# Kernel optimization log

Hardware: AMD Instinct MI355X
Metric: run time of the kernel (lower is better)

## Reference

```python
import jax, jax.numpy as jnp
import numpy as np

B, I, S, H, O = 128, 64, 2048, 128, 64


def setup_inputs() -> dict:
    key = jax.random.key(0)
    ks = jax.random.split(key, 9)
    sc = 0.1
    return {
        "x": jax.random.normal(ks[0], (B, I, S), dtype=jnp.float32),
        "Wx_out": jax.random.normal(ks[1], (I, 4 * H), dtype=jnp.float32) * sc,
        "Wh_out": jax.random.normal(ks[2], (H, 4 * H), dtype=jnp.float32) * sc,
        "b_out": jnp.zeros((4 * H,), dtype=jnp.float32),
        "Wx_in": jax.random.normal(ks[3], (H, 4 * H), dtype=jnp.float32) * sc,
        "Wh_in": jax.random.normal(ks[4], (H, 4 * H), dtype=jnp.float32) * sc,
        "b_in": jnp.zeros((4 * H,), dtype=jnp.float32),
        "W_lin": jax.random.normal(ks[5], (O, H), dtype=jnp.float32) * 0.01,
        "b_lin": jnp.zeros((O,), dtype=jnp.float32),
    }


def reference(x, Wx_out, Wh_out, b_out, Wx_in, Wh_in, b_in, W_lin, b_lin):
    # x: (B, I, S) -> permute(0,2,1) -> (B, S, I); scan over time axis.
    xs = jnp.transpose(x, (2, 0, 1))  # (S, B, I)
    h0 = jnp.zeros((x.shape[0], Wh_out.shape[0]), dtype=x.dtype)

    def step(carry, xt):
        h, c, cn = carry  # outer hidden, outer cell, inner cell
        gates = xt @ Wx_out + h @ Wh_out + b_out
        i, f, o, g = jnp.split(gates, 4, axis=-1)
        i, f, o = jax.nn.sigmoid(i), jax.nn.sigmoid(f), jax.nn.sigmoid(o)
        g = jnp.tanh(g)
        x_in = i * g          # inner LSTM input
        h_in = f * c          # inner LSTM hidden
        gi = x_in @ Wx_in + h_in @ Wh_in + b_in
        ii, fi, oi, gg = jnp.split(gi, 4, axis=-1)
        cn_new = jax.nn.sigmoid(fi) * cn + jax.nn.sigmoid(ii) * jnp.tanh(gg)
        c_new = jax.nn.sigmoid(oi) * jnp.tanh(cn_new)  # outer cell = inner hidden
        h_new = o * jnp.tanh(c_new)
        return (h_new, c_new, cn_new), h_new

    _, hs = jax.lax.scan(step, (h0, h0, h0), xs)  # hs: (S, B, H)
    hs = jnp.transpose(hs, (1, 0, 2))             # (B, S, H)
    return hs @ W_lin.T + b_lin                   # (B, S, O)
```

## Files before the change

### kernel.cpp

```cpp
#include <hip/hip_runtime.h>
#include <hip/hip_fp16.h>

#define BB 128
#define II 64
#define SS 2048
#define HH 128
#define GG 512
#define OO 64
#define TT 32
#define TCH 128
#define XPBYTES ((size_t)BB * SS * GG * 2)

typedef _Float16 f16x2 __attribute__((ext_vector_type(2)));
union F4H { float4 f4; f16x2 h[4]; };

__device__ __forceinline__ f16x2 pack2(float a, float b) {
    f16x2 r; r.x = (_Float16)a; r.y = (_Float16)b; return r;
}

__device__ __forceinline__ float dot2(f16x2 w, f16x2 v, float c) {
#if __has_builtin(__builtin_amdgcn_fdot2)
    return __builtin_amdgcn_fdot2(w, v, c, false);
#else
    return fmaf((float)w.x, (float)v.x, fmaf((float)w.y, (float)v.y, c));
#endif
}

__device__ __forceinline__ float sigm(float v) {
    return __builtin_amdgcn_rcpf(1.0f + __expf(-v));
}
__device__ __forceinline__ float tanh_f(float v) {
    float a = fabsf(v);
    float e = __expf(-2.0f * a);
    float r = (1.0f - e) * __builtin_amdgcn_rcpf(1.0f + e);
    return v < 0.0f ? -r : r;
}
__device__ __forceinline__ float tanh_c(float v) {
    return fmaf(2.0f, __builtin_amdgcn_rcpf(1.0f + __expf(-2.0f * v)), -1.0f);
}

template <int CTRL>
__device__ __forceinline__ float qdpp(float x) {
    return __int_as_float(__builtin_amdgcn_update_dpp(
        0, __float_as_int(x), CTRL, 0xF, 0xF, true));
}
#define QP_XOR3 0x1B
#define QP_BC0  0x00
#define QP_BC1  0x55
#define QP_BC2  0xAA

__global__ void __launch_bounds__(512)
xp_gemm(const float* __restrict__ x, const float* __restrict__ Wx_out,
        _Float16* __restrict__ xp)
{
    const int tc = blockIdx.x;
    const int b  = blockIdx.y;
    const int j  = threadIdx.x;
    const int t0 = tc * TCH;

    __shared__ __align__(16) f16x2 x2s[TCH][36];

    f16x2 w2[32];
#pragma unroll
    for (int c = 0; c < 32; ++c)
        w2[c] = pack2(Wx_out[(2 * c) * GG + j], Wx_out[(2 * c + 1) * GG + j]);

    const float* xrow = x + (size_t)b * II * SS;
    const int r = j >> 3;
#pragma unroll
    for (int rep = 0; rep < 4; ++rep) {
        const int u = (j & 7) + 8 * rep;
        const float4 v = *(const float4*)(xrow + (size_t)r * SS + t0 + 4 * u);
        const int c = r >> 1, half = r & 1;
        ((_Float16*)&x2s[4 * u + 0][c])[half] = (_Float16)v.x;
        ((_Float16*)&x2s[4 * u + 1][c])[half] = (_Float16)v.y;
        ((_Float16*)&x2s[4 * u + 2][c])[half] = (_Float16)v.z;
        ((_Float16*)&x2s[4 * u + 3][c])[half] = (_Float16)v.w;
    }
    __syncthreads();

    _Float16* xpo = xp + ((size_t)b * SS + t0) * GG + j;
#pragma unroll 4
    for (int tt = 0; tt < TCH; ++tt) {
        const float4* xr4 = (const float4*)&x2s[tt][0];
        float a0 = 0.f, a1 = 0.f;
#pragma unroll
        for (int q = 0; q < 8; ++q) {
            F4H u; u.f4 = xr4[q];
            a0 = dot2(w2[4 * q + 0], u.h[0], a0);
            a1 = dot2(w2[4 * q + 1], u.h[1], a1);
            a0 = dot2(w2[4 * q + 2], u.h[2], a0);
            a1 = dot2(w2[4 * q + 3], u.h[3], a1);
        }
        xpo[(size_t)tt * GG] = (_Float16)(a0 + a1);
    }
}

__global__ void __launch_bounds__(512)
nlstm_scan_xp(
    const _Float16* __restrict__ xp,
    const float* __restrict__ Wh_out, const float* __restrict__ b_out,
    const float* __restrict__ Wx_in, const float* __restrict__ Wh_in,
    const float* __restrict__ b_in,
    const float* __restrict__ W_lin, const float* __restrict__ b_lin,
    float* __restrict__ out)
{
    const int b = blockIdx.x;
    const int j = threadIdx.x;
    const int g = j & 3;
    const int m = j >> 2;
    const int col = g * 128 + m;

    __shared__ __align__(16) float4 whoL[16 * 512];
    __shared__ __align__(16) float4 wlf[16 * 66];
    __shared__ __align__(16) _Float16 hb[HH];
    __shared__ __align__(16) _Float16 xib[HH];
    __shared__ __align__(16) _Float16 hib[HH];

    f16x2 wxi[HH / 2], whi[HH / 2];
#pragma unroll
    for (int q = 0; q < HH / 2; ++q)
        wxi[q] = pack2(Wx_in[(2 * q) * GG + col], Wx_in[(2 * q + 1) * GG + col]);
#pragma unroll
    for (int q = 0; q < HH / 2; ++q)
        whi[q] = pack2(Wh_in[(2 * q) * GG + col], Wh_in[(2 * q + 1) * GG + col]);

#pragma unroll
    for (int c = 0; c < 16; ++c) {
        F4H u;
#pragma unroll
        for (int q = 0; q < 4; ++q)
            u.h[q] = pack2(Wh_out[(8 * c + 2 * q) * GG + col],
                           Wh_out[(8 * c + 2 * q + 1) * GG + col]);
        whoL[c * 512 + j] = u.f4;
    }

    const float bo = b_out[col];
    const float bi = b_in[col];
    const float kk = (g == 3) ? 2.0f : 1.0f;
    const float aa = (g == 3) ? 2.0f : 1.0f;
    const float cc = (g == 3) ? -1.0f : 0.0f;

    const int   pn = j >> 3;
    const int   ps = j & 7;
    const float bl = b_lin[pn];

#pragma unroll
    for (int r = 0; r < 2; ++r) {
        const int mm = r * 512 + j;
        const int c = mm >> 6, n = mm & 63;
        F4H u;
#pragma unroll
        for (int q = 0; q < 4; ++q)
            u.h[q] = pack2(W_lin[n * HH + 8 * c + 2 * q],
                           W_lin[n * HH + 8 * c + 2 * q + 1]);
        wlf[c * 66 + n] = u.f4;
    }

    if (j < HH) { hb[j] = (_Float16)0.f; xib[j] = (_Float16)0.f; hib[j] = (_Float16)0.f; }
    float c_reg = 0.f, cn_reg = 0.f;
    float o_all = 0.f;
    __syncthreads();

    const _Float16* xpr = xp + (size_t)b * SS * GG + col;
    float* orow = out + (size_t)b * SS * OO;
    const float4* hb4 = (const float4*)hb;
    const float4* xi4 = (const float4*)xib;
    const float4* hi4 = (const float4*)hib;

    _Float16 xpc = xpr[0];

#pragma unroll 1
    for (int t = 0; t < SS; ++t) {
        float a0 = bo + (float)xpc, a1 = 0.f, a2 = 0.f, a3 = 0.f;
#pragma unroll
        for (int c = 0; c < 16; ++c) {
            F4H hu; hu.f4 = hb4[c];
            F4H wu; wu.f4 = whoL[c * 512 + j];
            a0 = dot2(wu.h[0], hu.h[0], a0);
            a1 = dot2(wu.h[1], hu.h[1], a1);
            a2 = dot2(wu.h[2], hu.h[2], a2);
            a3 = dot2(wu.h[3], hu.h[3], a3);
        }
        const _Float16 xpn = xpr[(size_t)((t + 1) & (SS - 1)) * GG];
        const float accA = (a0 + a1) + (a2 + a3);
        const float v = fmaf(aa, sigm(kk * accA), cc);
        const float vg3 = qdpp<QP_XOR3>(v);
        o_all = qdpp<QP_BC2>(v);
        if (g == 0)      xib[m] = (_Float16)(v * vg3);
        else if (g == 1) hib[m] = (_Float16)(v * c_reg);
        __syncthreads();

        float c0 = bi, c1 = 0.f, c2 = 0.f, c3 = 0.f;
#pragma unroll
        for (int c = 0; c < 16; ++c) {
            F4H xu; xu.f4 = xi4[c];
            c0 = dot2(wxi[4 * c + 0], xu.h[0], c0);
            c1 = dot2(wxi[4 * c + 1], xu.h[1], c1);
            c2 = dot2(wxi[4 * c + 2], xu.h[2], c2);
            c3 = dot2(wxi[4 * c + 3], xu.h[3], c3);
        }
#pragma unroll
        for (int c = 0; c < 16; ++c) {
            F4H hu; hu.f4 = hi4[c];
            c0 = dot2(whi[4 * c + 0], hu.h[0], c0);
            c1 = dot2(whi[4 * c + 1], hu.h[1], c1);
            c2 = dot2(whi[4 * c + 2], hu.h[2], c2);
            c3 = dot2(whi[4 * c + 3], hu.h[3], c3);
        }
        const float accC = (c0 + c1) + (c2 + c3);
        const float u = fmaf(aa, sigm(kk * accC), cc);
        const float ug3 = qdpp<QP_XOR3>(u);
        const float p0  = u * ug3;
        const float P   = qdpp<QP_BC0>(p0);
        const float F   = qdpp<QP_BC1>(u);
        const float O   = qdpp<QP_BC2>(u);
        const float cn_new = fmaf(F, cn_reg, P);
        cn_reg = cn_new;
        const float c_new = O * tanh_c(cn_new);
        c_reg = c_new;
        const float h_new = o_all * tanh_c(c_new);
        if (g == 2) hb[m] = (_Float16)h_new;
        xpc = xpn;
        __syncthreads();

        float p = 0.f;
#pragma unroll
        for (int q = 0; q < 2; ++q) {
            const int c = 2 * ps + q;
            F4H hu; hu.f4 = hb4[c];
            F4H wu; wu.f4 = wlf[c * 66 + pn];
            p = dot2(wu.h[0], hu.h[0], p);
            p = dot2(wu.h[1], hu.h[1], p);
            p = dot2(wu.h[2], hu.h[2], p);
            p = dot2(wu.h[3], hu.h[3], p);
        }
        p += __shfl_down(p, 4, 8);
        p += __shfl_down(p, 2, 8);
        p += __shfl_down(p, 1, 8);
        if (ps == 0) orow[t * OO + pn] = p + bl;
    }
}

__global__ void
__attribute__((amdgpu_flat_work_group_size(512, 512)))
__attribute__((amdgpu_waves_per_eu(2, 2)))
nlstm_scan(
    const float* __restrict__ x,
    const float* __restrict__ Wx_out, const float* __restrict__ Wh_out,
    const float* __restrict__ b_out,
    const float* __restrict__ Wx_in, const float* __restrict__ Wh_in,
    const float* __restrict__ b_in,
    const float* __restrict__ W_lin, const float* __restrict__ b_lin,
    float* __restrict__ out)
{
    const int b = blockIdx.x;
    const int j = threadIdx.x;

    __shared__ __align__(16) float4 wxf[8 * 512];
    __shared__ __align__(16) float4 wlf[16 * 66];
    __shared__ float xt[2][II][TT + 1];
    __shared__ __align__(16) f16x2 xb[2][II / 2];
    __shared__ __align__(16) f16x2 hb[HH / 2];
    __shared__ __align__(16) f16x2 xib[HH / 2];
    __shared__ __align__(16) f16x2 hib[HH / 2];
    __shared__ float cb[HH];
    __shared__ float cnb[HH];
    __shared__ float actO[GG];
    __shared__ float actI[GG];

    f16x2 who[HH / 2], wxi[HH / 2], whi[HH / 2];
#pragma unroll
    for (int m = 0; m < HH / 2; ++m)
        who[m] = pack2(Wh_out[(2 * m) * GG + j], Wh_out[(2 * m + 1) * GG + j]);
#pragma unroll
    for (int m = 0; m < HH / 2; ++m)
        wxi[m] = pack2(Wx_in[(2 * m) * GG + j], Wx_in[(2 * m + 1) * GG + j]);
#pragma unroll
    for (int m = 0; m < HH / 2; ++m)
        whi[m] = pack2(Wh_in[(2 * m) * GG + j], Wh_in[(2 * m + 1) * GG + j]);

    const float bo = b_out[j];
    const float bi = b_in[j];
    const int   pn = j >> 3;
    const int   ps = j & 7;
    const float bl = b_lin[pn];

#pragma unroll
    for (int c = 0; c < 8; ++c) {
        F4H u;
#pragma unroll
        for (int q = 0; q < 4; ++q)
            u.h[q] = pack2(Wx_out[(8 * c + 2 * q) * GG + j],
                           Wx_out[(8 * c + 2 * q + 1) * GG + j]);
        wxf[c * 512 + j] = u.f4;
    }
#pragma unroll
    for (int r = 0; r < 2; ++r) {
        const int m = r * 512 + j;
        const int c = m >> 6, n = m & 63;
        F4H u;
#pragma unroll
        for (int q = 0; q < 4; ++q)
            u.h[q] = pack2(W_lin[n * HH + 8 * c + 2 * q],
                           W_lin[n * HH + 8 * c + 2 * q + 1]);
        wlf[c * 66 + n] = u.f4;
    }

    const float* xrow = x + (size_t)b * II * SS;
    float* orow = out + (size_t)b * SS * OO;

    {
        const int row = j >> 3, tc = j & 7;
        const float4 v = *(const float4*)(xrow + (size_t)row * SS + 4 * tc);
        float* dst = &xt[0][row][4 * tc];
        dst[0] = v.x; dst[1] = v.y; dst[2] = v.z; dst[3] = v.w;
    }
    if (j < HH / 2) hb[j] = pack2(0.f, 0.f);
    if (j < HH) { cb[j] = 0.f; cnb[j] = 0.f; }
    if (j >= 256 && j < 256 + 32) {
        const int m = j - 256;
        xb[0][m] = pack2(xrow[(2 * m) * SS], xrow[(2 * m + 1) * SS]);
    }
    __syncthreads();

    const float4* hb4 = (const float4*)hb;
    const float4* xi4 = (const float4*)xib;
    const float4* hi4 = (const float4*)hib;

#pragma unroll 1
    for (int t = 0; t < SS; ++t) {
        const float4* xcur = (const float4*)xb[t & 1];
        float a0 = bo, a1 = 0.f, a2 = 0.f, a3 = 0.f;
#pragma unroll
        for (int c = 0; c < 8; ++c) {
            F4H xu; xu.f4 = xcur[c];
            F4H wu; wu.f4 = wxf[c * 512 + j];
            a0 = dot2(wu.h[0], xu.h[0], a0);
            a1 = dot2(wu.h[1], xu.h[1], a1);
            a2 = dot2(wu.h[2], xu.h[2], a2);
            a3 = dot2(wu.h[3], xu.h[3], a3);
        }
#pragma unroll
        for (int c = 0; c < 16; ++c) {
            F4H hu; hu.f4 = hb4[c];
            a0 = dot2(who[4 * c + 0], hu.h[0], a0);
            a1 = dot2(who[4 * c + 1], hu.h[1], a1);
            a2 = dot2(who[4 * c + 2], hu.h[2], a2);
            a3 = dot2(who[4 * c + 3], hu.h[3], a3);
        }
        {
            const float acc = (a0 + a1) + (a2 + a3);
            actO[j] = (j < 384) ? sigm(acc) : tanh_f(acc);
        }
        __syncthreads();

        if (j < II) {
            xib[j] = pack2(actO[2 * j] * actO[384 + 2 * j],
                           actO[2 * j + 1] * actO[384 + 2 * j + 1]);
        } else if (j < II + HH / 2) {
            const int m = j - II;
            hib[m] = pack2(actO[HH + 2 * m] * cb[2 * m],
                           actO[HH + 2 * m + 1] * cb[2 * m + 1]);
        }
        __syncthreads();

        float c0 = bi, c1 = 0.f, c2 = 0.f, c3 = 0.f;
#pragma unroll
        for (int c = 0; c < 16; ++c) {
            F4H xu; xu.f4 = xi4[c];
            c0 = dot2(wxi[4 * c + 0], xu.h[0], c0);
            c1 = dot2(wxi[4 * c + 1], xu.h[1], c1);
            c2 = dot2(wxi[4 * c + 2], xu.h[2], c2);
            c3 = dot2(wxi[4 * c + 3], xu.h[3], c3);
        }
#pragma unroll
        for (int c = 0; c < 16; ++c) {
            F4H hu; hu.f4 = hi4[c];
            c0 = dot2(whi[4 * c + 0], hu.h[0], c0);
            c1 = dot2(whi[4 * c + 1], hu.h[1], c1);
            c2 = dot2(whi[4 * c + 2], hu.h[2], c2);
            c3 = dot2(whi[4 * c + 3], hu.h[3], c3);
        }
        {
            const float acc2 = (c0 + c1) + (c2 + c3);
            actI[j] = (j < 384) ? sigm(acc2) : tanh_f(acc2);
        }
        __syncthreads();

        const bool doTile = ((t & 31) == 30) && (t + 2 < SS);
        float4 xld; int Tn = 0;
        if (doTile) {
            Tn = (t + 2) >> 5;
            const int row = j >> 3, tc = j & 7;
            xld = *(const float4*)(xrow + (size_t)row * SS + TT * Tn + 4 * tc);
        }
        if (j < HH) {
            const float cn_new = actI[HH + j] * cnb[j] + actI[j] * actI[384 + j];
            const float c_new  = actI[2 * HH + j] * tanh_f(cn_new);
            const float h_new  = actO[2 * HH + j] * tanh_f(c_new);
            cnb[j] = cn_new;
            cb[j]  = c_new;
            ((_Float16*)hb)[j] = (_Float16)h_new;
        } else if (j < HH + 32) {
            const int m = j - HH;
            const int tn = t + 1;
            const int tbn = (tn >> 5) & 1, ttn = tn & 31;
            xb[tn & 1][m] = pack2(xt[tbn][2 * m][ttn],
                                  xt[tbn][2 * m + 1][ttn]);
        }
        if (doTile) {
            const int row = j >> 3, tc = j & 7;
            float* dst = &xt[Tn & 1][row][4 * tc];
            dst[0] = xld.x; dst[1] = xld.y; dst[2] = xld.z; dst[3] = xld.w;
        }
        __syncthreads();

        float p = 0.f;
#pragma unroll
        for (int q = 0; q < 2; ++q) {
            const int c = 2 * ps + q;
            F4H hu; hu.f4 = hb4[c];
            F4H wu; wu.f4 = wlf[c * 66 + pn];
            p = dot2(wu.h[0], hu.h[0], p);
            p = dot2(wu.h[1], hu.h[1], p);
            p = dot2(wu.h[2], hu.h[2], p);
            p = dot2(wu.h[3], hu.h[3], p);
        }
        p += __shfl_down(p, 4, 8);
        p += __shfl_down(p, 2, 8);
        p += __shfl_down(p, 1, 8);
        if (ps == 0) orow[t * OO + pn] = p + bl;
    }
}

extern "C" void kernel_launch(void* const* d_in, const int* in_sizes, int n_in,
                              void* d_out, int out_size, void* d_ws, size_t ws_size,
                              hipStream_t stream) {
    (void)in_sizes; (void)n_in; (void)out_size;
    const float* x      = (const float*)d_in[0];
    const float* Wx_out = (const float*)d_in[1];
    const float* Wh_out = (const float*)d_in[2];
    const float* b_out  = (const float*)d_in[3];
    const float* Wx_in  = (const float*)d_in[4];
    const float* Wh_in  = (const float*)d_in[5];
    const float* b_in   = (const float*)d_in[6];
    const float* W_lin  = (const float*)d_in[7];
    const float* b_lin  = (const float*)d_in[8];
    float* out = (float*)d_out;

    if (d_ws != nullptr && ws_size >= XPBYTES) {
        _Float16* xpw = (_Float16*)d_ws;
        xp_gemm<<<dim3(16, BB), dim3(512), 0, stream>>>(x, Wx_out, xpw);
        nlstm_scan_xp<<<dim3(BB), dim3(512), 0, stream>>>(
            xpw, Wh_out, b_out, Wx_in, Wh_in, b_in, W_lin, b_lin, out);
    } else {
        nlstm_scan<<<dim3(BB), dim3(512), 0, stream>>>(
            x, Wx_out, Wh_out, b_out, Wx_in, Wh_in, b_in, W_lin, b_lin, out);
    }
}
```

Baseline: 3.681 ms.

## Process two batch rows per block in recurrent scan to reuse weights

The scan kernel now handles two batch sequences per workgroup, launching half as many blocks. Each weight fragment loaded from LDS or registers is applied to both sequences' hidden states, and two independent dependency chains are interleaved to hide latency. It also swaps __syncthreads for a custom LDS-only waitcnt plus s_barrier. In exchange, only 64 blocks run on a GPU with far more CUs, and each serial step does roughly twice the ALU work, so per-step latency may grow.

```diff
diff --git a/kernel.cpp b/kernel.cpp
--- a/kernel.cpp
+++ b/kernel.cpp
@@ -49,6 +49,11 @@
 #define QP_BC1  0x55
 #define QP_BC2  0xAA
 
+__device__ __forceinline__ void lds_barrier() {
+    asm volatile("s_waitcnt lgkmcnt(0)" ::: "memory");
+    __builtin_amdgcn_s_barrier();
+}
+
 __global__ void __launch_bounds__(512)
 xp_gemm(const float* __restrict__ x, const float* __restrict__ Wx_out,
         _Float16* __restrict__ xp)
@@ -97,7 +102,7 @@
 }
 
 __global__ void __launch_bounds__(512)
-nlstm_scan_xp(
+nlstm_scan_xp2(
     const _Float16* __restrict__ xp,
     const float* __restrict__ Wh_out, const float* __restrict__ b_out,
     const float* __restrict__ Wx_in, const float* __restrict__ Wh_in,
@@ -105,17 +110,19 @@
     const float* __restrict__ W_lin, const float* __restrict__ b_lin,
     float* __restrict__ out)
 {
-    const int b = blockIdx.x;
-    const int j = threadIdx.x;
-    const int g = j & 3;
-    const int m = j >> 2;
+    const int blk = blockIdx.x;
+    const int b0  = 2 * blk;
+    const int b1  = 2 * blk + 1;
+    const int j   = threadIdx.x;
+    const int g   = j & 3;
+    const int m   = j >> 2;
     const int col = g * 128 + m;
 
     __shared__ __align__(16) float4 whoL[16 * 512];
     __shared__ __align__(16) float4 wlf[16 * 66];
-    __shared__ __align__(16) _Float16 hb[HH];
-    __shared__ __align__(16) _Float16 xib[HH];
-    __shared__ __align__(16) _Float16 hib[HH];
+    __shared__ __align__(16) _Float16 hb0s[HH],  hb1s[HH];
+    __shared__ __align__(16) _Float16 xib0[HH],  xib1[HH];
+    __shared__ __align__(16) _Float16 hib0[HH],  hib1[HH];
 
     f16x2 wxi[HH / 2], whi[HH / 2];
 #pragma unroll
@@ -157,88 +164,148 @@
         wlf[c * 66 + n] = u.f4;
     }
 
-    if (j < HH) { hb[j] = (_Float16)0.f; xib[j] = (_Float16)0.f; hib[j] = (_Float16)0.f; }
-    float c_reg = 0.f, cn_reg = 0.f;
-    float o_all = 0.f;
+    if (j < HH) {
+        hb0s[j] = (_Float16)0.f; hb1s[j] = (_Float16)0.f;
+        xib0[j] = (_Float16)0.f; xib1[j] = (_Float16)0.f;
+        hib0[j] = (_Float16)0.f; hib1[j] = (_Float16)0.f;
+    }
+    float c_reg0 = 0.f, cn_reg0 = 0.f, o_all0 = 0.f;
+    float c_reg1 = 0.f, cn_reg1 = 0.f, o_all1 = 0.f;
     __syncthreads();
 
-    const _Float16* xpr = xp + (size_t)b * SS * GG + col;
-    float* orow = out + (size_t)b * SS * OO;
-    const float4* hb4 = (const float4*)hb;
-    const float4* xi4 = (const float4*)xib;
-    const float4* hi4 = (const float4*)hib;
-
-    _Float16 xpc = xpr[0];
+    const _Float16* xpr0 = xp + (size_t)b0 * SS * GG + col;
+    const _Float16* xpr1 = xp + (size_t)b1 * SS * GG + col;
+    float* orow0 = out + (size_t)b0 * SS * OO;
+    float* orow1 = out + (size_t)b1 * SS * OO;
+    const float4* hb40 = (const float4*)hb0s;
+    const float4* hb41 = (const float4*)hb1s;
+    const float4* xi40 = (const float4*)xib0;
+    const float4* xi41 = (const float4*)xib1;
+    const float4* hi40 = (const float4*)hib0;
+    const float4* hi41 = (const float4*)hib1;
+
+    _Float16 xpc0 = xpr0[0];
+    _Float16 xpc1 = xpr1[0];
 
 #pragma unroll 1
     for (int t = 0; t < SS; ++t) {
-        float a0 = bo + (float)xpc, a1 = 0.f, a2 = 0.f, a3 = 0.f;
+        float aA0 = bo + (float)xpc0, aA1 = 0.f, aA2 = 0.f, aA3 = 0.f;
+        float aB0 = bo + (float)xpc1, aB1 = 0.f, aB2 = 0.f, aB3 = 0.f;
 #pragma unroll
         for (int c = 0; c < 16; ++c) {
-            F4H hu; hu.f4 = hb4[c];
             F4H wu; wu.f4 = whoL[c * 512 + j];
-            a0 = dot2(wu.h[0], hu.h[0], a0);
-            a1 = dot2(wu.h[1], hu.h[1], a1);
-            a2 = dot2(wu.h[2], hu.h[2], a2);
-            a3 = dot2(wu.h[3], hu.h[3], a3);
-        }
-        const _Float16 xpn = xpr[(size_t)((t + 1) & (SS - 1)) * GG];
-        const float accA = (a0 + a1) + (a2 + a3);
-        const float v = fmaf(aa, sigm(kk * accA), cc);
-        const float vg3 = qdpp<QP_XOR3>(v);
-        o_all = qdpp<QP_BC2>(v);
-        if (g == 0)      xib[m] = (_Float16)(v * vg3);
-        else if (g == 1) hib[m] = (_Float16)(v * c_reg);
-        __syncthreads();
-
-        float c0 = bi, c1 = 0.f, c2 = 0.f, c3 = 0.f;
+            F4H h0; h0.f4 = hb40[c];
+            F4H h1; h1.f4 = hb41[c];
+            aA0 = dot2(wu.h[0], h0.h[0], aA0);
+            aB0 = dot2(wu.h[0], h1.h[0], aB0);
+            aA1 = dot2(wu.h[1], h0.h[1], aA1);
+            aB1 = dot2(wu.h[1], h1.h[1], aB1);
+            aA2 = dot2(wu.h[2], h0.h[2], aA2);
+            aB2 = dot2(wu.h[2], h1.h[2], aB2);
+            aA3 = dot2(wu.h[3], h0.h[3], aA3);
+            aB3 = dot2(wu.h[3], h1.h[3], aB3);
+        }
+        const _Float16 xpn0 = xpr0[(size_t)((t + 1) & (SS - 1)) * GG];
+        const _Float16 xpn1 = xpr1[(size_t)((t + 1) & (SS - 1)) * GG];
+        const float accA = (aA0 + aA1) + (aA2 + aA3);
+        const float accB = (aB0 + aB1) + (aB2 + aB3);
+        const float vA = fmaf(aa, sigm(kk * accA), cc);
+        const float vB = fmaf(aa, sigm(kk * accB), cc);
+        const float vg3A = qdpp<QP_XOR3>(vA);
+        const float vg3B = qdpp<QP_XOR3>(vB);
+        o_all0 = qdpp<QP_BC2>(vA);
+        o_all1 = qdpp<QP_BC2>(vB);
+        if (g == 0) {
+            xib0[m] = (_Float16)(vA * vg3A);
+            xib1[m] = (_Float16)(vB * vg3B);
+        } else if (g == 1) {
+            hib0[m] = (_Float16)(vA * c_reg0);
+            hib1[m] = (_Float16)(vB * c_reg1);
+        }
+        lds_barrier();
+
+        float cA0 = bi, cA1 = 0.f, cA2 = 0.f, cA3 = 0.f;
+        float cB0 = bi, cB1 = 0.f, cB2 = 0.f, cB3 = 0.f;
 #pragma unroll
         for (int c = 0; c < 16; ++c) {
-            F4H xu; xu.f4 = xi4[c];
-            c0 = dot2(wxi[4 * c + 0], xu.h[0], c0);
-            c1 = dot2(wxi[4 * c + 1], xu.h[1], c1);
-            c2 = dot2(wxi[4 * c + 2], xu.h[2], c2);
-            c3 = dot2(wxi[4 * c + 3], xu.h[3], c3);
+            F4H x0; x0.f4 = xi40[c];
+            F4H x1; x1.f4 = xi41[c];
+            cA0 = dot2(wxi[4 * c + 0], x0.h[0], cA0);
+            cB0 = dot2(wxi[4 * c + 0], x1.h[0], cB0);
+            cA1 = dot2(wxi[4 * c + 1], x0.h[1], cA1);
+            cB1 = dot2(wxi[4 * c + 1], x1.h[1], cB1);
+            cA2 = dot2(wxi[4 * c + 2], x0.h[2], cA2);
+            cB2 = dot2(wxi[4 * c + 2], x1.h[2], cB2);
+            cA3 = dot2(wxi[4 * c + 3], x0.h[3], cA3);
+            cB3 = dot2(wxi[4 * c + 3], x1.h[3], cB3);
         }
 #pragma unroll
         for (int c = 0; c < 16; ++c) {
-            F4H hu; hu.f4 = hi4[c];
-            c0 = dot2(whi[4 * c + 0], hu.h[0], c0);
-            c1 = dot2(whi[4 * c + 1], hu.h[1], c1);
-            c2 = dot2(whi[4 * c + 2], hu.h[2], c2);
-            c3 = dot2(whi[4 * c + 3], hu.h[3], c3);
-        }
-        const float accC = (c0 + c1) + (c2 + c3);
-        const float u = fmaf(aa, sigm(kk * accC), cc);
-        const float ug3 = qdpp<QP_XOR3>(u);
-        const float p0  = u * ug3;
-        const float P   = qdpp<QP_BC0>(p0);
-        const float F   = qdpp<QP_BC1>(u);
-        const float O   = qdpp<QP_BC2>(u);
-        const float cn_new = fmaf(F, cn_reg, P);
-        cn_reg = cn_new;
-        const float c_new = O * tanh_c(cn_new);
-        c_reg = c_new;
-        const float h_new = o_all * tanh_c(c_new);
-        if (g == 2) hb[m] = (_Float16)h_new;
-        xpc = xpn;
-        __syncthreads();
-
-        float p = 0.f;
+            F4H h0; h0.f4 = hi40[c];
+            F4H h1; h1.f4 = hi41[c];
+            cA0 = dot2(whi[4 * c + 0], h0.h[0], cA0);
+            cB0 = dot2(whi[4 * c + 0], h1.h[0], cB0);
+            cA1 = dot2(whi[4 * c + 1], h0.h[1], cA1);
+            cB1 = dot2(whi[4 * c + 1], h1.h[1], cB1);
+            cA2 = dot2(whi[4 * c + 2], h0.h[2], cA2);
+            cB2 = dot2(whi[4 * c + 2], h1.h[2], cB2);
+            cA3 = dot2(whi[4 * c + 3], h0.h[3], cA3);
+            cB3 = dot2(whi[4 * c + 3], h1.h[3], cB3);
+        }
+        const float accCA = (cA0 + cA1) + (cA2 + cA3);
+        const float accCB = (cB0 + cB1) + (cB2 + cB3);
+        const float uA = fmaf(aa, sigm(kk * accCA), cc);
+        const float uB = fmaf(aa, sigm(kk * accCB), cc);
+        {
+            const float ug3A = qdpp<QP_XOR3>(uA);
+            const float ug3B = qdpp<QP_XOR3>(uB);
+            const float p0A = uA * ug3A;
+            const float p0B = uB * ug3B;
+            const float PA = qdpp<QP_BC0>(p0A);
+            const float PB = qdpp<QP_BC0>(p0B);
+            const float FA = qdpp<QP_BC1>(uA);
+            const float FB = qdpp<QP_BC1>(uB);
+            const float OA = qdpp<QP_BC2>(uA);
+            const float OB = qdpp<QP_BC2>(uB);
+            const float cnA = fmaf(FA, cn_reg0, PA);
+            const float cnB = fmaf(FB, cn_reg1, PB);
+            cn_reg0 = cnA; cn_reg1 = cnB;
+            const float cA = OA * tanh_c(cnA);
+            const float cB = OB * tanh_c(cnB);
+            c_reg0 = cA; c_reg1 = cB;
+            const float hA = o_all0 * tanh_c(cA);
+            const float hB = o_all1 * tanh_c(cB);
+            if (g == 2) { hb0s[m] = (_Float16)hA; hb1s[m] = (_Float16)hB; }
+        }
+        xpc0 = xpn0; xpc1 = xpn1;
+        lds_barrier();
+
+        float pA = 0.f, pB = 0.f;
 #pragma unroll
         for (int q = 0; q < 2; ++q) {
             const int c = 2 * ps + q;
-            F4H hu; hu.f4 = hb4[c];
             F4H wu; wu.f4 = wlf[c * 66 + pn];
-            p = dot2(wu.h[0], hu.h[0], p);
-            p = dot2(wu.h[1], hu.h[1], p);
-            p = dot2(wu.h[2], hu.h[2], p);
-            p = dot2(wu.h[3], hu.h[3], p);
-        }
-        p += __shfl_down(p, 4, 8);
-        p += __shfl_down(p, 2, 8);
-        p += __shfl_down(p, 1, 8);
-        if (ps == 0) orow[t * OO + pn] = p + bl;
+            F4H h0; h0.f4 = hb40[c];
+            F4H h1; h1.f4 = hb41[c];
+            pA = dot2(wu.h[0], h0.h[0], pA);
+            pB = dot2(wu.h[0], h1.h[0], pB);
+            pA = dot2(wu.h[1], h0.h[1], pA);
+            pB = dot2(wu.h[1], h1.h[1], pB);
+            pA = dot2(wu.h[2], h0.h[2], pA);
+            pB = dot2(wu.h[2], h1.h[2], pB);
+            pA = dot2(wu.h[3], h0.h[3], pA);
+            pB = dot2(wu.h[3], h1.h[3], pB);
+        }
+        pA += __shfl_down(pA, 4, 8);
+        pB += __shfl_down(pB, 4, 8);
+        pA += __shfl_down(pA, 2, 8);
+        pB += __shfl_down(pB, 2, 8);
+        pA += __shfl_down(pA, 1, 8);
+        pB += __shfl_down(pB, 1, 8);
+        if (ps == 0) {
+            orow0[t * OO + pn] = pA + bl;
+            orow1[t * OO + pn] = pB + bl;
+        }
     }
 }
 
@@ -452,7 +519,7 @@
     if (d_ws != nullptr && ws_size >= XPBYTES) {
         _Float16* xpw = (_Float16*)d_ws;
         xp_gemm<<<dim3(16, BB), dim3(512), 0, stream>>>(x, Wx_out, xpw);
-        nlstm_scan_xp<<<dim3(BB), dim3(512), 0, stream>>>(
+        nlstm_scan_xp2<<<dim3(BB / 2), dim3(512), 0, stream>>>(
             xpw, Wh_out, b_out, Wx_in, Wh_in, b_in, W_lin, b_lin, out);
     } else {
         nlstm_scan<<<dim3(BB), dim3(512), 0, stream>>>(
```

New measurement: 6.868 ms. 86.6% more time.
